# Optimization experiments

Hardware: AMD Instinct MI355X
Metric: run time of the kernel (lower is better)

Reference implementation:

```python
import jax, jax.numpy as jnp
import numpy as np
from jax.scipy.special import logsumexp

TAU = 0.07
LAMBDA_LL = 1.0
LAMBDA_GL = 0.5
LAMBDA_SMOOTH = 0.1
NEG_INF = -jnp.inf


def setup_inputs() -> dict:
    key = jax.random.key(0)
    k1, k2, k3, k4 = jax.random.split(key, 4)
    B, L, D, K = 16, 32, 256, 131072
    return {
        "z_t": jax.random.normal(k1, (B, L, D), dtype=jnp.float32),
        "g": jax.random.normal(k2, (B, D), dtype=jnp.float32),
        "va_values": jax.random.uniform(k3, (B, L, 2), dtype=jnp.float32),
        "memory_queue": jax.random.normal(k4, (K, D), dtype=jnp.float32),
    }


def _combined_loss(z_t, g, memory_queue):
    B, L, D = z_t.shape
    N = B * L
    z = z_t.reshape(N, D)

    # ---- Global-Local loss: anchor g[b], positive z_t[b,t], negatives = frames of other clips + queue
    sim_gz = (g @ z.T) / TAU                      # [B, N]
    pos_gl = sim_gz.reshape(B, B, L)[jnp.arange(B), jnp.arange(B)]  # [B, L]
    col_batch = jnp.arange(N) // L                # batch id of each frame column
    neg_gl = jnp.where(col_batch[None, :] == jnp.arange(B)[:, None], NEG_INF, sim_gz)  # [B, N]
    q_gl = (g @ memory_queue.T) / TAU             # [B, K]
    lse_neg_gl = jnp.logaddexp(logsumexp(neg_gl, axis=1), logsumexp(q_gl, axis=1))     # [B]
    loss_gl = jnp.mean(jnp.logaddexp(pos_gl, lse_neg_gl[:, None]) - pos_gl)

    # ---- Local-Local loss: anchor (b,t), positive (b,t+1), negatives = all other frames + queue
    anchor_idx = (jnp.arange(B)[:, None] * L + jnp.arange(L - 1)[None, :]).reshape(-1)  # [M]
    M = anchor_idx.shape[0]
    sim_zz = (z @ z.T) / TAU                      # [N, N]
    rows = sim_zz[anchor_idx]                     # [M, N]
    pos_ll = sim_zz[anchor_idx, anchor_idx + 1]   # [M]
    r = jnp.arange(M)
    neg_rows = rows.at[r, anchor_idx].set(NEG_INF).at[r, anchor_idx + 1].set(NEG_INF)
    q_ll = (z[anchor_idx] @ memory_queue.T) / TAU  # [M, K] -- dominant memory traffic
    lse_neg_ll = jnp.logaddexp(logsumexp(neg_rows, axis=1), logsumexp(q_ll, axis=1))
    loss_ll = jnp.mean(jnp.logaddexp(pos_ll, lse_neg_ll) - pos_ll)
    # NOTE: the VA-derived positive weight in the original code is applied after
    # the logits are built, so it has no effect on the loss; reproduced faithfully.

    # ---- Smoothness loss
    diff = z_t[:, 1:, :] - z_t[:, :-1, :]
    loss_smooth = jnp.mean(jnp.sum(diff * diff, axis=-1))

    total = LAMBDA_LL * loss_ll + LAMBDA_GL * loss_gl + LAMBDA_SMOOTH * loss_smooth
    return total


def reference(z_t, g, va_values, memory_queue):
    # va_values is unused by the effective math (see note in _combined_loss)
    return _combined_loss(z_t, g, memory_queue)
```

## Files before the change

kernel.cpp:

```cpp
#include <hip/hip_runtime.h>
#include <hip/hip_bf16.h>

#define D_ 256
#define NROWS_Z 512
#define NROWS 528
#define KQ 131072
#define SCALE_A 20.6099291041f
#define INV_SCALE_A (1.0f / SCALE_A)
#define LN2 0.6931471805599453f

typedef __attribute__((ext_vector_type(8))) short short8;
typedef __attribute__((ext_vector_type(4))) float f32x4;

__device__ __forceinline__ float exp2fast(float x) {
  float r; asm("v_exp_f32 %0, %1" : "=v"(r) : "v"(x)); return r;
}
__device__ __forceinline__ float log2fast(float x) {
  float r; asm("v_log_f32 %0, %1" : "=v"(r) : "v"(x)); return r;
}

__device__ __forceinline__ short bf16r(float x) {
  union { float f; unsigned u; } c; c.f = x;
  unsigned r = (c.u + 0x7fffu + ((c.u >> 16) & 1u)) >> 16;
  return (short)r;
}

__device__ __forceinline__ unsigned cvt2fp8(float a, float b) {
  unsigned r;
  asm("v_cvt_pk_fp8_f32 %0, %1, %2" : "=v"(r) : "v"(a), "v"(b));
  return r & 0xFFFFu;
}

__device__ __forceinline__ void merge_ms(float& m, float& s, float m2, float s2) {
  float mm = fmaxf(m, m2);
  s = s * exp2fast(m - mm) + s2 * exp2fast(m2 - mm);
  m = mm;
}

__device__ __forceinline__ void upd(float& m, float& s, float v) {
  float d = v - m;
  if (__builtin_expect(__any(d > 8.f), 0)) {
    const float mn = fmaxf(m, v);
    s *= exp2fast(m - mn);
    m = mn; d = v - m;
  }
  s += exp2fast(d);
}

__global__ void prep_kernel(const float* __restrict__ z, const float* __restrict__ g,
                            short* __restrict__ Abf, char* __restrict__ Abf8,
                            float* __restrict__ smoothp) {
  const int r = blockIdx.x, d = threadIdx.x;
  __shared__ float vals[256];
  __shared__ float red[4];
  const float v = (r < NROWS_Z) ? z[r * D_ + d] : g[(r - NROWS_Z) * D_ + d];
  const float vs = v * SCALE_A;
  Abf[r * D_ + d] = bf16r(vs);
  vals[d] = vs;
  float acc = 0.f;
  if (r < NROWS_Z && (r & 31) != 31) { const float dv = z[(r + 1) * D_ + d] - v; acc = dv * dv; }
#pragma unroll
  for (int mask = 1; mask < 64; mask <<= 1) acc += __shfl_xor(acc, mask);
  if ((d & 63) == 0) red[d >> 6] = acc;
  __syncthreads();
  if (d < 64) {
    const float4 q = *(const float4*)(vals + d * 4);
    const unsigned w = cvt2fp8(q.x, q.y) | (cvt2fp8(q.z, q.w) << 16);
    *(unsigned*)(Abf8 + r * D_ + d * 4) = w;
  }
  if (d == 0 && r < NROWS_Z) smoothp[r] = red[0] + red[1] + red[2] + red[3];
}

__global__ __launch_bounds__(512, 2) void big_kernel(
    const float* __restrict__ queue, const char* __restrict__ Abf8,
    float2* __restrict__ zpart, float2* __restrict__ gpart,
    int nchunk, int subt) {
  const int tid = threadIdx.x, blk = blockIdx.x;
  const int wid = tid >> 6, lane = tid & 63;
  const int l15 = lane & 15, l4 = lane >> 4;
  const int qrows = KQ / nchunk;

  __shared__ __align__(16) char qs[2][16 * 256];
  __shared__ float2 gbuf[8][16];

  long afrag[4][8];
#pragma unroll
  for (int s = 0; s < 4; ++s) {
    const char* base = Abf8 + (wid * 64 + s * 16 + l15) * D_ + l4 * 8;
#pragma unroll
    for (int k = 0; k < 8; ++k) afrag[s][k] = *(const long*)(base + k * 32);
  }
  const char* gBbase = Abf8 + (NROWS_Z + l15) * D_ + l4 * 8;

  float mz[4][4], sz[4][4];
#pragma unroll
  for (int s = 0; s < 4; ++s)
#pragma unroll
    for (int r = 0; r < 4; ++r) { mz[s][r] = -1e30f; sz[s][r] = 0.f; }
  float mg = -1e30f, sg = 0.f;

  const int srow = tid >> 5;
  const int sslot = tid & 31;
  const int woff = srow * D_ + ((sslot ^ srow) << 3);
  const float* qbase = queue + (size_t)(blk * qrows + srow) * D_ + sslot * 8;

  const f32x4 fz = {0.f, 0.f, 0.f, 0.f};

#define STAGE(BUF)                                                                    \
  {                                                                                   \
    const unsigned w0 = cvt2fp8(fa0.x, fa0.y) | (cvt2fp8(fa0.z, fa0.w) << 16);        \
    const unsigned w1 = cvt2fp8(fa1.x, fa1.y) | (cvt2fp8(fa1.z, fa1.w) << 16);        \
    *(uint2*)(qs[BUF] + woff) = make_uint2(w0, w1);                                   \
  }

#define COMPUTE(BUF, ST)                                                              \
  {                                                                                   \
    const char* qb = qs[BUF];                                                         \
    f32x4 acc0 = fz, acc1 = fz, acc2 = fz, acc3 = fz;                                 \
    _Pragma("unroll")                                                                 \
    for (int kk = 0; kk < 8; ++kk) {                                                  \
      const long bf = *(const long*)(qb + l15 * D_ + (((kk * 4 + l4) ^ l15) << 3));   \
      acc0 = __builtin_amdgcn_mfma_f32_16x16x32_fp8_fp8(afrag[0][kk], bf, acc0, 0, 0, 0); \
      acc1 = __builtin_amdgcn_mfma_f32_16x16x32_fp8_fp8(afrag[1][kk], bf, acc1, 0, 0, 0); \
      acc2 = __builtin_amdgcn_mfma_f32_16x16x32_fp8_fp8(afrag[2][kk], bf, acc2, 0, 0, 0); \
      acc3 = __builtin_amdgcn_mfma_f32_16x16x32_fp8_fp8(afrag[3][kk], bf, acc3, 0, 0, 0); \
    }                                                                                 \
    _Pragma("unroll")                                                                 \
    for (int r = 0; r < 4; ++r) {                                                     \
      upd(mz[0][r], sz[0][r], acc0[r]);                                               \
      upd(mz[1][r], sz[1][r], acc1[r]);                                               \
      upd(mz[2][r], sz[2][r], acc2[r]);                                               \
      upd(mz[3][r], sz[3][r], acc3[r]);                                               \
    }                                                                                 \
    if ((((ST) & 7)) == wid) {                                                        \
      f32x4 accg = fz;                                                                \
      _Pragma("unroll")                                                               \
      for (int kk = 0; kk < 8; ++kk) {                                                \
        const long bf = *(const long*)(qb + l15 * D_ + (((kk * 4 + l4) ^ l15) << 3)); \
        const long gb = *(const long*)(gBbase + kk * 32);                             \
        accg = __builtin_amdgcn_mfma_f32_16x16x32_fp8_fp8(bf, gb, accg, 0, 0, 0);     \
      }                                                                               \
      _Pragma("unroll")                                                               \
      for (int r = 0; r < 4; ++r) upd(mg, sg, accg[r]);                               \
    }                                                                                 \
  }

  float4 fa0 = *(const float4*)qbase;
  float4 fa1 = *(const float4*)(qbase + 4);
  STAGE(0)
  __syncthreads();

  for (int st = 0; st < subt; st += 2) {
    {
      const float* qp = qbase + (size_t)(st + 1) * (16 * D_);
      fa0 = *(const float4*)qp;
      fa1 = *(const float4*)(qp + 4);
    }
    COMPUTE(0, st)
    STAGE(1)
    __syncthreads();

    if (st + 2 < subt) {
      const float* qp = qbase + (size_t)(st + 2) * (16 * D_);
      fa0 = *(const float4*)qp;
      fa1 = *(const float4*)(qp + 4);
    }
    COMPUTE(1, st + 1)
    if (st + 2 < subt) STAGE(0)
    __syncthreads();
  }

#pragma unroll
  for (int s = 0; s < 4; ++s)
#pragma unroll
    for (int r = 0; r < 4; ++r) {
#pragma unroll
      for (int mask = 1; mask < 16; mask <<= 1) {
        const float om = __shfl_xor(mz[s][r], mask);
        const float os = __shfl_xor(sz[s][r], mask);
        merge_ms(mz[s][r], sz[s][r], om, os);
      }
    }
  if (l15 == 0) {
#pragma unroll
    for (int s = 0; s < 4; ++s)
#pragma unroll
      for (int r = 0; r < 4; ++r) {
        const int row = wid * 64 + s * 16 + l4 * 4 + r;
        zpart[row * nchunk + blk] = make_float2(mz[s][r], sz[s][r]);
      }
  }

#pragma unroll
  for (int mask = 16; mask < 64; mask <<= 1) {
    const float om = __shfl_xor(mg, mask);
    const float os = __shfl_xor(sg, mask);
    merge_ms(mg, sg, om, os);
  }
  if (lane < 16) gbuf[wid][l15] = make_float2(mg, sg);
  __syncthreads();
  if (tid < 16) {
    float m = gbuf[0][tid].x, s = gbuf[0][tid].y;
    for (int w = 1; w < 8; ++w) merge_ms(m, s, gbuf[w][tid].x, gbuf[w][tid].y);
    gpart[tid * nchunk + blk] = make_float2(m, s);
  }
}

__global__ __launch_bounds__(512) void zmm_kernel(
    const short* __restrict__ Abf,
    float2* __restrict__ zcol, float* __restrict__ posll, float* __restrict__ posgl) {
  const int tid = threadIdx.x;
  const int wid = tid >> 6, lane = tid & 63;
  const int l15 = lane & 15, l4 = lane >> 4;
  const int r0 = blockIdx.x * 16;

  short8 af[8];
#pragma unroll
  for (int k = 0; k < 8; ++k)
    af[k] = *(const short8*)(Abf + (r0 + l15) * D_ + l4 * 8 + k * 32);

  float m[4], s[4];
#pragma unroll
  for (int r = 0; r < 4; ++r) { m[r] = -1e30f; s[r] = 0.f; }

  for (int st = 0; st < 4; ++st) {
    const int c0 = wid * 64 + st * 16;
    const f32x4 fz = {0.f, 0.f, 0.f, 0.f};
    f32x4 acc = fz;
#pragma unroll
    for (int k = 0; k < 8; ++k) {
      const short8 bq = *(const short8*)(Abf + (c0 + l15) * D_ + l4 * 8 + k * 32);
      acc = __builtin_amdgcn_mfma_f32_16x16x32_bf16(af[k], bq, acc, 0, 0, 0);
    }
#pragma unroll
    for (int r = 0; r < 4; ++r) {
      const int row = r0 + l4 * 4 + r;
      const int col = c0 + l15;
      const float v = acc[r] * INV_SCALE_A;
      bool masked;
      if (r0 < NROWS_Z) {
        if (col == row + 1) posll[row] = v * LN2;
        masked = (col == row) || (col == row + 1);
      } else {
        const int b = row - NROWS_Z;
        const bool own = ((col >> 5) == b);
        if (own) posgl[col] = v * LN2;
        masked = own;
      }
      if (!masked) upd(m[r], s[r], v);
    }
  }
#pragma unroll
  for (int r = 0; r < 4; ++r) {
#pragma unroll
    for (int mask = 1; mask < 16; mask <<= 1) {
      const float om = __shfl_xor(m[r], mask);
      const float os = __shfl_xor(s[r], mask);
      merge_ms(m[r], s[r], om, os);
    }
  }
  __shared__ float2 lds[8][16];
  if (l15 == 0) {
#pragma unroll
    for (int r = 0; r < 4; ++r) lds[wid][l4 * 4 + r] = make_float2(m[r], s[r]);
  }
  __syncthreads();
  if (tid < 16) {
    float mm = lds[0][tid].x, ss = lds[0][tid].y;
    for (int w = 1; w < 8; ++w) merge_ms(mm, ss, lds[w][tid].x, lds[w][tid].y);
    zcol[r0 + tid] = make_float2(mm, ss);
  }
}

__global__ void reduce_kernel(const float2* __restrict__ zpart, const float2* __restrict__ gpart,
                              const float2* __restrict__ zcol, float* __restrict__ lse_row,
                              int nchunk) {
  const int r = blockIdx.x, tid = threadIdx.x;
  const float2 p = (r < NROWS_Z) ? zpart[r * nchunk + tid] : gpart[(r - NROWS_Z) * nchunk + tid];
  float m = p.x, s = p.y;
  __shared__ float2 red[8];
#pragma unroll
  for (int mask = 1; mask < 64; mask <<= 1) {
    const float om = __shfl_xor(m, mask);
    const float os = __shfl_xor(s, mask);
    merge_ms(m, s, om, os);
  }
  if ((tid & 63) == 0) red[tid >> 6] = make_float2(m, s);
  __syncthreads();
  if (tid == 0) {
    const int nw = blockDim.x >> 6;
    for (int w = 1; w < nw; ++w) merge_ms(m, s, red[w].x, red[w].y);
    const float2 zc = zcol[r];
    merge_ms(m, s, zc.x, zc.y);
    lse_row[r] = LN2 * (m + log2fast(s));
  }
}

__global__ void final_kernel(const float* __restrict__ lse_row, const float* __restrict__ posll,
                             const float* __restrict__ posgl, const float* __restrict__ smoothp,
                             float* __restrict__ out) {
  const int tid = threadIdx.x;
  float a_ll = 0.f, a_gl = 0.f, a_sm = 0.f;
  for (int i = tid; i < 496; i += 256) {
    const int b = i / 31, t = i - b * 31;
    const int a = b * 32 + t;
    const float pos = posll[a], lse = lse_row[a];
    const float d = lse - pos;
    a_ll += (d > 0.f) ? d + log1pf(__expf(-d)) : log1pf(__expf(d));
  }
  for (int i = tid; i < 512; i += 256) {
    const float pos = posgl[i], lse = lse_row[NROWS_Z + (i >> 5)];
    const float d = lse - pos;
    a_gl += (d > 0.f) ? d + log1pf(__expf(-d)) : log1pf(__expf(d));
  }
  for (int i = tid; i < 512; i += 256) a_sm += smoothp[i];

  __shared__ float red[4];
  float sums[3] = {a_ll, a_gl, a_sm};
  float tot[3];
  for (int j = 0; j < 3; ++j) {
    float v = sums[j];
#pragma unroll
    for (int mask = 1; mask < 64; mask <<= 1) v += __shfl_xor(v, mask);
    __syncthreads();
    if ((tid & 63) == 0) red[tid >> 6] = v;
    __syncthreads();
    tot[j] = red[0] + red[1] + red[2] + red[3];
  }
  if (tid == 0)
    out[0] = tot[0] / 496.f + 0.5f * (tot[1] / 512.f) + 0.1f * (tot[2] / 496.f);
}

extern "C" void kernel_launch(void* const* d_in, const int* in_sizes, int n_in,
                              void* d_out, int out_size, void* d_ws, size_t ws_size,
                              hipStream_t stream) {
  const float* z = (const float*)d_in[0];
  const float* g = (const float*)d_in[1];
  const float* queue = (const float*)d_in[3];
  float* out = (float*)d_out;
  char* ws = (char*)d_ws;

  const size_t offA = 0;
  const size_t offA8 = 270336;
  const size_t offZpart = offA8 + 135168;
  auto need = [&](int nc) -> size_t {
    return offZpart + (size_t)512 * nc * 8 + (size_t)16 * nc * 8 + 4224 + 2048 + 2048 + 2048 + 2112;
  };
  const int nchunk = (ws_size >= need(512)) ? 512 : 256;
  const int subt = (KQ / nchunk) / 16;

  const size_t offGpart = offZpart + (size_t)512 * nchunk * 8;
  const size_t offZcol = offGpart + (size_t)16 * nchunk * 8;
  const size_t offPosll = offZcol + 4224;
  const size_t offPosgl = offPosll + 2048;
  const size_t offSm = offPosgl + 2048;
  const size_t offLse = offSm + 2048;

  short* Abf = (short*)(ws + offA);
  char* Abf8 = (char*)(ws + offA8);
  float2* zpart = (float2*)(ws + offZpart);
  float2* gpart = (float2*)(ws + offGpart);
  float2* zcol = (float2*)(ws + offZcol);
  float* posll = (float*)(ws + offPosll);
  float* posgl = (float*)(ws + offPosgl);
  float* smoothp = (float*)(ws + offSm);
  float* lse_row = (float*)(ws + offLse);

  prep_kernel<<<NROWS, 256, 0, stream>>>(z, g, Abf, Abf8, smoothp);
  big_kernel<<<nchunk, 512, 0, stream>>>(queue, Abf8, zpart, gpart, nchunk, subt);
  zmm_kernel<<<33, 512, 0, stream>>>(Abf, zcol, posll, posgl);
  reduce_kernel<<<NROWS, nchunk, 0, stream>>>(zpart, gpart, zcol, lse_row, nchunk);
  final_kernel<<<1, 256, 0, stream>>>(lse_row, posll, posgl, smoothp, out);
}
```

Measured before the change: 118.3 us.

## Split z rows across two block groups with larger double-buffered queue tiles

The main kernel now launches 512 blocks: 256 queue chunks of 512 rows each, times two row groups of 256 z rows. Each wave holds only two A fragments instead of four, which cuts register pressure. The queue is staged in 32-row fp8 tiles using 64-byte per-thread loads, a new swizzle and explicit barriers. The cost is that every queue chunk is read from global memory and converted to fp8 twice, once per row group, which doubles load and conversion work unless the cache absorbs the repeat reads. The chunk count is now fixed at 256 and the workspace-size fallback is removed.

Result: faster. 103.3 us (-12.7%).

```diff
diff --git a/kernel.cpp b/kernel.cpp
--- a/kernel.cpp
+++ b/kernel.cpp
@@ -5,6 +5,9 @@
 #define NROWS_Z 512
 #define NROWS 528
 #define KQ 131072
+#define NCHUNK 256
+#define QR 512
+#define PH 16
 #define SCALE_A 20.6099291041f
 #define INV_SCALE_A (1.0f / SCALE_A)
 #define LN2 0.6931471805599453f
@@ -73,105 +76,104 @@
 
 __global__ __launch_bounds__(512, 2) void big_kernel(
     const float* __restrict__ queue, const char* __restrict__ Abf8,
-    float2* __restrict__ zpart, float2* __restrict__ gpart,
-    int nchunk, int subt) {
-  const int tid = threadIdx.x, blk = blockIdx.x;
+    float2* __restrict__ zpart, float2* __restrict__ gpart) {
+  const int tid = threadIdx.x;
+  const int chunk = blockIdx.x & 255;
+  const int rg = blockIdx.x >> 8;
   const int wid = tid >> 6, lane = tid & 63;
   const int l15 = lane & 15, l4 = lane >> 4;
-  const int qrows = KQ / nchunk;
-
-  __shared__ __align__(16) char qs[2][16 * 256];
+  const int l4h = l4 >> 1;
+  const int h8 = (l4 & 1) << 3;
+
+  __shared__ __align__(16) char qs[2][32 * 256];
   __shared__ float2 gbuf[8][16];
 
-  long afrag[4][8];
-#pragma unroll
-  for (int s = 0; s < 4; ++s) {
-    const char* base = Abf8 + (wid * 64 + s * 16 + l15) * D_ + l4 * 8;
+  long afrag[2][8];
+#pragma unroll
+  for (int s = 0; s < 2; ++s) {
+    const char* base = Abf8 + (rg * 256 + wid * 32 + s * 16 + l15) * D_ + l4 * 8;
 #pragma unroll
     for (int k = 0; k < 8; ++k) afrag[s][k] = *(const long*)(base + k * 32);
   }
   const char* gBbase = Abf8 + (NROWS_Z + l15) * D_ + l4 * 8;
 
-  float mz[4][4], sz[4][4];
-#pragma unroll
-  for (int s = 0; s < 4; ++s)
+  float mz[2][4], sz[2][4];
+#pragma unroll
+  for (int s = 0; s < 2; ++s)
 #pragma unroll
     for (int r = 0; r < 4; ++r) { mz[s][r] = -1e30f; sz[s][r] = 0.f; }
   float mg = -1e30f, sg = 0.f;
-
-  const int srow = tid >> 5;
-  const int sslot = tid & 31;
-  const int woff = srow * D_ + ((sslot ^ srow) << 3);
-  const float* qbase = queue + (size_t)(blk * qrows + srow) * D_ + sslot * 8;
+  const bool dog = (rg == 0);
+
+  const int srow = tid >> 4;
+  const int scol = tid & 15;
+  const int woff = srow * D_ + ((scol ^ (srow & 15)) << 4);
+  const float* qbase = queue + (size_t)(chunk * QR + srow) * D_ + scol * 16;
 
   const f32x4 fz = {0.f, 0.f, 0.f, 0.f};
 
-#define STAGE(BUF)                                                                    \
-  {                                                                                   \
-    const unsigned w0 = cvt2fp8(fa0.x, fa0.y) | (cvt2fp8(fa0.z, fa0.w) << 16);        \
-    const unsigned w1 = cvt2fp8(fa1.x, fa1.y) | (cvt2fp8(fa1.z, fa1.w) << 16);        \
-    *(uint2*)(qs[BUF] + woff) = make_uint2(w0, w1);                                   \
-  }
-
-#define COMPUTE(BUF, ST)                                                              \
-  {                                                                                   \
-    const char* qb = qs[BUF];                                                         \
-    f32x4 acc0 = fz, acc1 = fz, acc2 = fz, acc3 = fz;                                 \
-    _Pragma("unroll")                                                                 \
-    for (int kk = 0; kk < 8; ++kk) {                                                  \
-      const long bf = *(const long*)(qb + l15 * D_ + (((kk * 4 + l4) ^ l15) << 3));   \
+  float4 fa0, fa1, fa2, fa3, fb0, fb1, fb2, fb3;
+
+#define LOADP(S0, S1, S2, S3, P)                                    \
+  { const float4* qp = (const float4*)(qbase + (size_t)(P) * (32 * D_)); \
+    S0 = qp[0]; S1 = qp[1]; S2 = qp[2]; S3 = qp[3]; }
+
+#define CVTW(S0, S1, S2, S3, BUF)                                   \
+  { const unsigned w0 = cvt2fp8(S0.x, S0.y) | (cvt2fp8(S0.z, S0.w) << 16); \
+    const unsigned w1 = cvt2fp8(S1.x, S1.y) | (cvt2fp8(S1.z, S1.w) << 16); \
+    const unsigned w2 = cvt2fp8(S2.x, S2.y) | (cvt2fp8(S2.z, S2.w) << 16); \
+    const unsigned w3 = cvt2fp8(S3.x, S3.y) | (cvt2fp8(S3.z, S3.w) << 16); \
+    *(uint4*)(qs[BUF] + woff) = make_uint4(w0, w1, w2, w3); }
+
+#define PBAR()                                                      \
+  { asm volatile("s_waitcnt lgkmcnt(0)" ::: "memory");              \
+    __builtin_amdgcn_sched_barrier(0);                              \
+    __builtin_amdgcn_s_barrier(); }
+
+#define CHALF(BUF, H, SIDX)                                         \
+  { const char* qb = qs[BUF] + (H) * 16 * D_ + l15 * D_ + h8;       \
+    f32x4 acc0 = fz, acc1 = fz;                                     \
+    _Pragma("unroll")                                               \
+    for (int kk = 0; kk < 8; ++kk) {                                \
+      const long bf = *(const long*)(qb + ((((kk * 2 + l4h)) ^ l15) << 4)); \
       acc0 = __builtin_amdgcn_mfma_f32_16x16x32_fp8_fp8(afrag[0][kk], bf, acc0, 0, 0, 0); \
       acc1 = __builtin_amdgcn_mfma_f32_16x16x32_fp8_fp8(afrag[1][kk], bf, acc1, 0, 0, 0); \
-      acc2 = __builtin_amdgcn_mfma_f32_16x16x32_fp8_fp8(afrag[2][kk], bf, acc2, 0, 0, 0); \
-      acc3 = __builtin_amdgcn_mfma_f32_16x16x32_fp8_fp8(afrag[3][kk], bf, acc3, 0, 0, 0); \
-    }                                                                                 \
-    _Pragma("unroll")                                                                 \
-    for (int r = 0; r < 4; ++r) {                                                     \
-      upd(mz[0][r], sz[0][r], acc0[r]);                                               \
-      upd(mz[1][r], sz[1][r], acc1[r]);                                               \
-      upd(mz[2][r], sz[2][r], acc2[r]);                                               \
-      upd(mz[3][r], sz[3][r], acc3[r]);                                               \
-    }                                                                                 \
-    if ((((ST) & 7)) == wid) {                                                        \
-      f32x4 accg = fz;                                                                \
-      _Pragma("unroll")                                                               \
-      for (int kk = 0; kk < 8; ++kk) {                                                \
-        const long bf = *(const long*)(qb + l15 * D_ + (((kk * 4 + l4) ^ l15) << 3)); \
-        const long gb = *(const long*)(gBbase + kk * 32);                             \
-        accg = __builtin_amdgcn_mfma_f32_16x16x32_fp8_fp8(bf, gb, accg, 0, 0, 0);     \
-      }                                                                               \
-      _Pragma("unroll")                                                               \
-      for (int r = 0; r < 4; ++r) upd(mg, sg, accg[r]);                               \
-    }                                                                                 \
-  }
-
-  float4 fa0 = *(const float4*)qbase;
-  float4 fa1 = *(const float4*)(qbase + 4);
-  STAGE(0)
-  __syncthreads();
-
-  for (int st = 0; st < subt; st += 2) {
-    {
-      const float* qp = qbase + (size_t)(st + 1) * (16 * D_);
-      fa0 = *(const float4*)qp;
-      fa1 = *(const float4*)(qp + 4);
-    }
-    COMPUTE(0, st)
-    STAGE(1)
-    __syncthreads();
-
-    if (st + 2 < subt) {
-      const float* qp = qbase + (size_t)(st + 2) * (16 * D_);
-      fa0 = *(const float4*)qp;
-      fa1 = *(const float4*)(qp + 4);
-    }
-    COMPUTE(1, st + 1)
-    if (st + 2 < subt) STAGE(0)
-    __syncthreads();
-  }
-
-#pragma unroll
-  for (int s = 0; s < 4; ++s)
+    }                                                               \
+    _Pragma("unroll")                                               \
+    for (int r = 0; r < 4; ++r) { upd(mz[0][r], sz[0][r], acc0[r]); upd(mz[1][r], sz[1][r], acc1[r]); } \
+    if (dog && (((SIDX) & 7) == wid)) {                             \
+      f32x4 accg = fz;                                              \
+      _Pragma("unroll")                                             \
+      for (int kk = 0; kk < 8; ++kk) {                              \
+        const long bf = *(const long*)(qb + ((((kk * 2 + l4h)) ^ l15) << 4)); \
+        const long gb = *(const long*)(gBbase + kk * 32);           \
+        accg = __builtin_amdgcn_mfma_f32_16x16x32_fp8_fp8(bf, gb, accg, 0, 0, 0); \
+      }                                                             \
+      _Pragma("unroll")                                             \
+      for (int r = 0; r < 4; ++r) upd(mg, sg, accg[r]);             \
+    } }
+
+  LOADP(fa0, fa1, fa2, fa3, 0)
+  LOADP(fb0, fb1, fb2, fb3, 1)
+  CVTW(fa0, fa1, fa2, fa3, 0)
+  PBAR()
+
+  for (int i = 0; i < PH / 2; ++i) {
+    const int t = 2 * i;
+    if (t + 2 < PH) LOADP(fa0, fa1, fa2, fa3, t + 2)
+    CHALF(0, 0, t * 2)
+    CHALF(0, 1, t * 2 + 1)
+    CVTW(fb0, fb1, fb2, fb3, 1)
+    PBAR()
+    if (t + 3 < PH) LOADP(fb0, fb1, fb2, fb3, t + 3)
+    CHALF(1, 0, t * 2 + 2)
+    CHALF(1, 1, t * 2 + 3)
+    if (t + 2 < PH) CVTW(fa0, fa1, fa2, fa3, 0)
+    PBAR()
+  }
+
+#pragma unroll
+  for (int s = 0; s < 2; ++s)
 #pragma unroll
     for (int r = 0; r < 4; ++r) {
 #pragma unroll
@@ -183,26 +185,28 @@
     }
   if (l15 == 0) {
 #pragma unroll
-    for (int s = 0; s < 4; ++s)
+    for (int s = 0; s < 2; ++s)
 #pragma unroll
       for (int r = 0; r < 4; ++r) {
-        const int row = wid * 64 + s * 16 + l4 * 4 + r;
-        zpart[row * nchunk + blk] = make_float2(mz[s][r], sz[s][r]);
+        const int row = rg * 256 + wid * 32 + s * 16 + l4 * 4 + r;
+        zpart[row * NCHUNK + chunk] = make_float2(mz[s][r], sz[s][r]);
       }
   }
 
-#pragma unroll
-  for (int mask = 16; mask < 64; mask <<= 1) {
-    const float om = __shfl_xor(mg, mask);
-    const float os = __shfl_xor(sg, mask);
-    merge_ms(mg, sg, om, os);
-  }
-  if (lane < 16) gbuf[wid][l15] = make_float2(mg, sg);
-  __syncthreads();
-  if (tid < 16) {
-    float m = gbuf[0][tid].x, s = gbuf[0][tid].y;
-    for (int w = 1; w < 8; ++w) merge_ms(m, s, gbuf[w][tid].x, gbuf[w][tid].y);
-    gpart[tid * nchunk + blk] = make_float2(m, s);
+  if (dog) {
+#pragma unroll
+    for (int mask = 16; mask < 64; mask <<= 1) {
+      const float om = __shfl_xor(mg, mask);
+      const float os = __shfl_xor(sg, mask);
+      merge_ms(mg, sg, om, os);
+    }
+    if (lane < 16) gbuf[wid][l15] = make_float2(mg, sg);
+    __syncthreads();
+    if (tid < 16) {
+      float m = gbuf[0][tid].x, s = gbuf[0][tid].y;
+      for (int w = 1; w < 8; ++w) merge_ms(m, s, gbuf[w][tid].x, gbuf[w][tid].y);
+      gpart[tid * NCHUNK + chunk] = make_float2(m, s);
+    }
   }
 }
 
@@ -273,12 +277,11 @@
 }
 
 __global__ void reduce_kernel(const float2* __restrict__ zpart, const float2* __restrict__ gpart,
-                              const float2* __restrict__ zcol, float* __restrict__ lse_row,
-                              int nchunk) {
+                              const float2* __restrict__ zcol, float* __restrict__ lse_row) {
   const int r = blockIdx.x, tid = threadIdx.x;
-  const float2 p = (r < NROWS_Z) ? zpart[r * nchunk + tid] : gpart[(r - NROWS_Z) * nchunk + tid];
+  const float2 p = (r < NROWS_Z) ? zpart[r * NCHUNK + tid] : gpart[(r - NROWS_Z) * NCHUNK + tid];
   float m = p.x, s = p.y;
-  __shared__ float2 red[8];
+  __shared__ float2 red[4];
 #pragma unroll
   for (int mask = 1; mask < 64; mask <<= 1) {
     const float om = __shfl_xor(m, mask);
@@ -288,8 +291,7 @@
   if ((tid & 63) == 0) red[tid >> 6] = make_float2(m, s);
   __syncthreads();
   if (tid == 0) {
-    const int nw = blockDim.x >> 6;
-    for (int w = 1; w < nw; ++w) merge_ms(m, s, red[w].x, red[w].y);
+    for (int w = 1; w < 4; ++w) merge_ms(m, s, red[w].x, red[w].y);
     const float2 zc = zcol[r];
     merge_ms(m, s, zc.x, zc.y);
     lse_row[r] = LN2 * (m + log2fast(s));
@@ -343,14 +345,8 @@
   const size_t offA = 0;
   const size_t offA8 = 270336;
   const size_t offZpart = offA8 + 135168;
-  auto need = [&](int nc) -> size_t {
-    return offZpart + (size_t)512 * nc * 8 + (size_t)16 * nc * 8 + 4224 + 2048 + 2048 + 2048 + 2112;
-  };
-  const int nchunk = (ws_size >= need(512)) ? 512 : 256;
-  const int subt = (KQ / nchunk) / 16;
-
-  const size_t offGpart = offZpart + (size_t)512 * nchunk * 8;
-  const size_t offZcol = offGpart + (size_t)16 * nchunk * 8;
+  const size_t offGpart = offZpart + 1048576;
+  const size_t offZcol = offGpart + 32768;
   const size_t offPosll = offZcol + 4224;
   const size_t offPosgl = offPosll + 2048;
   const size_t offSm = offPosgl + 2048;
@@ -367,8 +363,8 @@
   float* lse_row = (float*)(ws + offLse);
 
   prep_kernel<<<NROWS, 256, 0, stream>>>(z, g, Abf, Abf8, smoothp);
-  big_kernel<<<nchunk, 512, 0, stream>>>(queue, Abf8, zpart, gpart, nchunk, subt);
+  big_kernel<<<512, 512, 0, stream>>>(queue, Abf8, zpart, gpart);
   zmm_kernel<<<33, 512, 0, stream>>>(Abf, zcol, posll, posgl);
-  reduce_kernel<<<NROWS, nchunk, 0, stream>>>(zpart, gpart, zcol, lse_row, nchunk);
+  reduce_kernel<<<NROWS, NCHUNK, 0, stream>>>(zpart, gpart, zcol, lse_row);
   final_kernel<<<1, 256, 0, stream>>>(lse_row, posll, posgl, smoothp, out);
 }
```
